# Kernel tuning notes

Hardware: AMD Instinct MI355X
Metric: run time of the kernel (lower is better)

The kernel has to match this reference:

```python
import jax, jax.numpy as jnp
import numpy as np

G, N_PER_G, V, H, DIN, DOUT, E = 1024, 64, 32, 128, 128, 10, 1048576
N = G * N_PER_G


def _lin(key, fan_in, fan_out):
    k1, k2 = jax.random.split(key)
    s = 1.0 / np.sqrt(fan_in)
    return (jax.random.uniform(k1, (fan_in, fan_out), jnp.float32, -s, s),
            jax.random.uniform(k2, (fan_out,), jnp.float32, -s, s))


def setup_inputs() -> dict:
    key = jax.random.key(0)
    ks = jax.random.split(key, 16)
    x = jax.random.normal(ks[0], (N, DIN), jnp.float32)
    # random edges constrained within each graph's contiguous node block
    gid = jax.random.randint(ks[1], (E,), 0, G)
    src = gid * N_PER_G + jax.random.randint(ks[2], (E,), 0, N_PER_G)
    dst = gid * N_PER_G + jax.random.randint(ks[3], (E,), 0, N_PER_G)
    edge_index = jnp.stack([src, dst]).astype(jnp.int64)
    batch = jnp.repeat(jnp.arange(G, dtype=jnp.int64), N_PER_G)
    edge_weights = jnp.ones((G, N_PER_G, V), jnp.float32) / V  # uniform init
    vemb = jax.random.normal(ks[4], (G, V, H), jnp.float32)
    vemb = vemb / jnp.linalg.norm(vemb, axis=-1, keepdims=True)
    W_emb, b_emb = _lin(ks[5], DIN, H)
    W_gcn, b_gcn = _lin(ks[6], H, H)
    aff_W1, aff_b1 = _lin(ks[7], H, H)
    aff_W2, aff_b2 = _lin(ks[8], H, H)
    vn_W1, vn_b1 = _lin(ks[9], H, H)
    vn_W2, vn_b2 = _lin(ks[10], H, H)
    mlp_W1, mlp_b1 = _lin(ks[11], H, H)
    mlp_W2, mlp_b2 = _lin(ks[12], H, DOUT)
    return dict(x=x, edge_index=edge_index, batch=batch, edge_weights=edge_weights,
                vemb=vemb, W_emb=W_emb, b_emb=b_emb, W_gcn=W_gcn, b_gcn=b_gcn,
                aff_W1=aff_W1, aff_b1=aff_b1, aff_W2=aff_W2, aff_b2=aff_b2,
                vn_W1=vn_W1, vn_b1=vn_b1, vn_W2=vn_W2, vn_b2=vn_b2,
                mlp_W1=mlp_W1, mlp_b1=mlp_b1, mlp_W2=mlp_W2, mlp_b2=mlp_b2)


def reference(x, edge_index, batch, edge_weights, vemb, W_emb, b_emb, W_gcn, b_gcn,
              aff_W1, aff_b1, aff_W2, aff_b2, vn_W1, vn_b1, vn_W2, vn_b2,
              mlp_W1, mlp_b1, mlp_W2, mlp_b2):
    n_nodes = x.shape[0]
    g, n, v = edge_weights.shape
    h = x @ W_emb + b_emb                                   # node embedding
    # GCNConv with self-loops and symmetric normalization
    hw = h @ W_gcn
    sl = jnp.arange(n_nodes)
    s = jnp.concatenate([edge_index[0], sl])
    d = jnp.concatenate([edge_index[1], sl])
    deg = jax.ops.segment_sum(jnp.ones_like(d, dtype=h.dtype), d, num_segments=n_nodes)
    inv = jax.lax.rsqrt(jnp.maximum(deg, 1.0))
    msg = hw[s] * (inv[s] * inv[d])[:, None]                # [E+N, H]
    h = jax.nn.relu(jax.ops.segment_sum(msg, d, num_segments=n_nodes) + b_gcn)
    # affinity MLP
    aff = jax.nn.relu(h @ aff_W1 + aff_b1) @ aff_W2 + aff_b2
    hg = h.reshape(g, n, -1)
    affg = aff.reshape(g, n, -1)
    # attention vs fixed normalized virtual-node embeddings
    att = jnp.einsum('gnh,gvh->gnv', affg, vemb) / jnp.sqrt(jnp.asarray(hg.shape[-1], h.dtype))
    ew = edge_weights * (1.0 + jax.nn.sigmoid(att))
    rs = ew.sum(axis=-1, keepdims=True)
    ew = ew / jnp.where(rs == 0, 1.0, rs)                   # row-normalize
    vn = jnp.einsum('gnv,gnh->gvh', ew, hg)                 # weighted scatter-pool
    vn = jax.nn.relu(vn @ vn_W1 + vn_b1) @ vn_W2 + vn_b2
    gf = vn.mean(axis=1)                                    # [G, H]
    return jax.nn.relu(gf @ mlp_W1 + mlp_b1) @ mlp_W2 + mlp_b2
```

## Files before the change

### kernel.cpp

```cpp
#include <hip/hip_runtime.h>
#include <hip/hip_bf16.h>
#include <cstddef>


#define EDGES 1048576
#define CAP 2048
#define SR 136
#define ST 72

typedef __attribute__((ext_vector_type(8))) short short8;
typedef __attribute__((ext_vector_type(4))) float f32x4;
typedef __hip_bfloat16 bf;
struct __align__(8) bf4 { bf v[4]; };

__global__ __launch_bounds__(256) void edge_hist(const int* __restrict__ ei,
                                                 unsigned* __restrict__ H)
{
    __shared__ unsigned lh[1024];
    int tid = threadIdx.x, b = blockIdx.x;
    for (int t = tid; t < 1024; t += 256) lh[t] = 0;
    __syncthreads();
    int base = b * 4096;
#pragma unroll 4
    for (int t = 0; t < 16; ++t) {
        int s = ei[base + t * 256 + tid];
        atomicAdd(&lh[s >> 6], 1u);
    }
    __syncthreads();
    for (int t = tid; t < 1024; t += 256) H[b * 1024 + t] = lh[t];
}

__global__ __launch_bounds__(256) void scan_conv(
    unsigned* __restrict__ H, unsigned* __restrict__ Tot,
    const float* __restrict__ w0, const float* __restrict__ w1,
    const float* __restrict__ w2, const float* __restrict__ w3,
    const float* __restrict__ w4, const float* __restrict__ w5,
    bf* __restrict__ outw)
{
    int b = blockIdx.x;
    if (b < 256) {
        int wv = threadIdx.x >> 6, lane = threadIdx.x & 63;
        int g = b * 4 + wv;
        unsigned v[4];
#pragma unroll
        for (int c = 0; c < 4; ++c) v[c] = H[(c * 64 + lane) * 1024 + g];
        unsigned run = 0;
#pragma unroll
        for (int c = 0; c < 4; ++c) {
            unsigned s = v[c];
            unsigned incl = s;
#pragma unroll
            for (int d = 1; d < 64; d <<= 1) {
                unsigned t = __shfl_up(incl, d);
                if (lane >= d) incl += t;
            }
            H[(c * 64 + lane) * 1024 + g] = run + (incl - s);
            run += __shfl(incl, 63);
        }
        if (lane == 0) Tot[g] = run;
    } else {
        int idx = (b - 256) * 256 + threadIdx.x;
        int n = idx >> 7, k = idx & 127;
        int off = (((n >> 4) * 4 + (k >> 5)) * 512) + (n & 15) * 32 + (k & 31);
        const float* srcs[6] = { w0, w1, w2, w3, w4, w5 };
#pragma unroll
        for (int m = 0; m < 6; ++m) {
            float vv = (m == 3) ? srcs[m][n * 128 + k] : srcs[m][k * 128 + n];
            outw[m * 16384 + off] = __float2bfloat16(vv);
        }
    }
}

__global__ __launch_bounds__(256) void edge_scatter(const int* __restrict__ ei,
                                                    const unsigned* __restrict__ H,
                                                    unsigned short* __restrict__ sorted)
{
    __shared__ unsigned lh[1024];
    __shared__ unsigned hrow[1024];
    int tid = threadIdx.x, b = blockIdx.x;
    for (int t = tid; t < 1024; t += 256) { lh[t] = 0; hrow[t] = H[b * 1024 + t]; }
    __syncthreads();
    int base = b * 4096;
    for (int t = 0; t < 16; ++t) {
        int e = base + t * 256 + tid;
        int s = ei[e], d = ei[EDGES + e];
        int g = s >> 6;
        unsigned r = atomicAdd(&lh[g], 1u);
        unsigned o = hrow[g] + r;
        if (o < (unsigned)CAP)
            sorted[(unsigned)g * CAP + o] = (unsigned short)(((d & 63) << 6) | (s & 63));
    }
}

__device__ __forceinline__ void loadB(const bf* __restrict__ gW, int wv, int l15,
                                      int kofs, short8* B)
{
#pragma unroll
    for (int nt = 0; nt < 2; ++nt)
#pragma unroll
        for (int ks = 0; ks < 4; ++ks)
            B[nt * 4 + ks] = *(const short8*)(gW + (((wv * 2 + nt) * 4 + ks) * 512)
                                              + l15 * 32 + kofs);
}

template<int MT, int KS, int SA>
__device__ __forceinline__ void mmaAB(const bf* sA, int rowA, int l15, int kofs,
                                      const short8* B, f32x4 (*acc)[2])
{
#pragma unroll
    for (int ks = 0; ks < KS; ++ks) {
        short8 a[MT];
#pragma unroll
        for (int m = 0; m < MT; ++m)
            a[m] = *(const short8*)(sA + (rowA + m * 16 + l15) * SA + ks * 32 + kofs);
#pragma unroll
        for (int m = 0; m < MT; ++m)
#pragma unroll
            for (int nt = 0; nt < 2; ++nt)
                acc[m][nt] = __builtin_amdgcn_mfma_f32_16x16x32_bf16(
                    a[m], B[nt * 4 + ks], acc[m][nt], 0, 0, 0);
    }
}

template<int MT, int KS, int SA, int SB>
__device__ __forceinline__ void mmaABlds(const bf* sA, int rowA, const bf* sB, int rowB,
                                         int l15, int kofs, f32x4 (*acc)[2])
{
#pragma unroll
    for (int ks = 0; ks < KS; ++ks) {
        short8 bb[2];
#pragma unroll
        for (int nt = 0; nt < 2; ++nt)
            bb[nt] = *(const short8*)(sB + (rowB + nt * 16 + l15) * SB + ks * 32 + kofs);
        short8 a[MT];
#pragma unroll
        for (int m = 0; m < MT; ++m)
            a[m] = *(const short8*)(sA + (rowA + m * 16 + l15) * SA + ks * 32 + kofs);
#pragma unroll
        for (int m = 0; m < MT; ++m)
#pragma unroll
            for (int nt = 0; nt < 2; ++nt)
                acc[m][nt] = __builtin_amdgcn_mfma_f32_16x16x32_bf16(
                    a[m], bb[nt], acc[m][nt], 0, 0, 0);
    }
}

__global__ __launch_bounds__(256, 2) void fused_graph(
    const float* __restrict__ x, const float* __restrict__ edge_w,
    const float* __restrict__ vemb, const bf* __restrict__ gWb,
    const float* __restrict__ b_emb,  const float* __restrict__ b_gcn,
    const float* __restrict__ aff_b1, const float* __restrict__ aff_b2,
    const float* __restrict__ vn_b1,  const float* __restrict__ vn_b2,
    const float* __restrict__ mlp_W1, const float* __restrict__ mlp_b1,
    const float* __restrict__ mlp_W2, const float* __restrict__ mlp_b2,
    const unsigned short* __restrict__ sorted,
    const unsigned* __restrict__ Tot,
    float* __restrict__ out)
{
    __shared__ __align__(16) bf sRM1[64 * SR];
    __shared__ __align__(16) bf sRM2[64 * SR];
    __shared__ __align__(16) bf sT1 [128 * ST];
    __shared__ __align__(16) bf sT2 [128 * ST];
    __shared__ __align__(16) bf sAdj[64 * ST];
    __shared__ float sInv[64];
    __shared__ float sBatt[32];

    unsigned* cnt = (unsigned*)sT1;
    bf* sVemb = sAdj;
    bf* sS    = sT1;
    bf* sEwnT = sT1 + 4608;
    float* sT2f = (float*)sT2;

    const int tid = threadIdx.x;
    const int g = blockIdx.x;
    const int wv = tid >> 6;
    const int lane = tid & 63;
    const int l15 = lane & 15;
    const int q = lane >> 4;
    const int kofs = q * 8;

    short8 Bp[8], Bn[8];
    loadB(gWb, wv, l15, kofs, Bp);
    loadB(gWb + 16384, wv, l15, kofs, Bn);
    float4 xreg[8];
    const float4* gx = (const float4*)(x + (size_t)g * 8192);
#pragma unroll
    for (int t = 0; t < 8; ++t) xreg[t] = gx[tid + t * 256];
    float4 vreg[4];
    const float4* gv = (const float4*)(vemb + (size_t)g * 4096);
#pragma unroll
    for (int t = 0; t < 4; ++t) vreg[t] = gv[tid + t * 256];
    float ewreg[2][4];
#pragma unroll
    for (int nt = 0; nt < 2; ++nt)
#pragma unroll
        for (int r = 0; r < 4; ++r)
            ewreg[nt][r] = edge_w[(size_t)g * 2048 + (wv * 16 + q * 4 + r) * 32
                                  + nt * 16 + l15];
    float bias_e[2], bias_g[2], bias_a1[2], bias_v1[2], bias_v2[2];
#pragma unroll
    for (int nt = 0; nt < 2; ++nt) {
        int n = wv * 32 + nt * 16 + l15;
        bias_e[nt] = b_emb[n];  bias_g[nt] = b_gcn[n]; bias_a1[nt] = aff_b1[n];
        bias_v1[nt] = vn_b1[n]; bias_v2[nt] = vn_b2[n];
    }
    unsigned ecnt = min(Tot[g], (unsigned)CAP);
    unsigned ebase = (unsigned)g * CAP;

#pragma unroll
    for (int t = 0; t < 4; ++t) cnt[tid * 4 + t] = 0u;
    __syncthreads();
    for (unsigned i = tid; i < ecnt; i += 256) {
        unsigned w = sorted[ebase + i];
        unsigned d = w >> 6, s = w & 63u;
        atomicAdd(&cnt[d * 16 + (s >> 2)], 1u << ((s & 3u) * 8));
    }
#pragma unroll
    for (int t = 0; t < 8; ++t) {
        int i = tid + t * 256;
        int row = i >> 5, c4 = i & 31;
        float4 w = xreg[t];
        bf4 tt;
        tt.v[0] = __float2bfloat16(w.x); tt.v[1] = __float2bfloat16(w.y);
        tt.v[2] = __float2bfloat16(w.z); tt.v[3] = __float2bfloat16(w.w);
        *(bf4*)(sRM1 + row * SR + c4 * 4) = tt;
    }
    __syncthreads();
    {
        int r = tid >> 2, q4 = tid & 3;
        float rs = 0.f;
#pragma unroll
        for (int t = 0; t < 4; ++t) {
            unsigned wd = cnt[r * 16 + q4 * 4 + t];
#pragma unroll
            for (int j = 0; j < 4; ++j) {
                int s = (q4 * 4 + t) * 4 + j;
                float v = (float)((wd >> (j * 8)) & 255u) + (s == r ? 1.f : 0.f);
                rs += v;
                sAdj[r * ST + s] = __float2bfloat16(v);
            }
        }
        rs += __shfl_xor(rs, 1);
        rs += __shfl_xor(rs, 2);
        if (q4 == 0) sInv[r] = rsqrtf(rs);
    }
    __syncthreads();

    {
        f32x4 acc[4][2] = {};
        mmaAB<4, 4, SR>(sRM1, 0, l15, kofs, Bp, acc);
        loadB(gWb + 2 * 16384, wv, l15, kofs, Bp);
#pragma unroll
        for (int m = 0; m < 4; ++m)
#pragma unroll
            for (int nt = 0; nt < 2; ++nt)
#pragma unroll
                for (int r = 0; r < 4; ++r)
                    sRM2[(m * 16 + q * 4 + r) * SR + wv * 32 + nt * 16 + l15] =
                        __float2bfloat16(acc[m][nt][r] + bias_e[nt]);
    }
    __syncthreads();

    {
        f32x4 acc[4][2] = {};
        mmaAB<4, 4, SR>(sRM2, 0, l15, kofs, Bn, acc);
        loadB(gWb + 3 * 16384, wv, l15, kofs, Bn);
#pragma unroll
        for (int m = 0; m < 4; ++m)
#pragma unroll
            for (int nt = 0; nt < 2; ++nt) {
                bf4 tv;
#pragma unroll
                for (int r = 0; r < 4; ++r)
                    tv.v[r] = __float2bfloat16(acc[m][nt][r] * sInv[m * 16 + q * 4 + r]);
                *(bf4*)(sT1 + (wv * 32 + nt * 16 + l15) * ST + m * 16 + q * 4) = tv;
            }
    }
    __syncthreads();

    {
        f32x4 acc[4][2] = {};
        mmaABlds<4, 2, ST, ST>(sAdj, 0, sT1, wv * 32, l15, kofs, acc);
#pragma unroll
        for (int m = 0; m < 4; ++m)
#pragma unroll
            for (int nt = 0; nt < 2; ++nt) {
                bf4 tv;
#pragma unroll
                for (int r = 0; r < 4; ++r) {
                    float v = fmaxf(acc[m][nt][r] * sInv[m * 16 + q * 4 + r] + bias_g[nt], 0.f);
                    sRM1[(m * 16 + q * 4 + r) * SR + wv * 32 + nt * 16 + l15] = __float2bfloat16(v);
                    tv.v[r] = __float2bfloat16(v);
                }
                *(bf4*)(sT2 + (wv * 32 + nt * 16 + l15) * ST + m * 16 + q * 4) = tv;
            }
    }
    __syncthreads();

    {
#pragma unroll
        for (int t = 0; t < 4; ++t) {
            int i = tid + t * 256;
            int v = i >> 5, o4 = i & 31;
            float4 w = vreg[t];
            bf4 tt;
            tt.v[0] = __float2bfloat16(w.x); tt.v[1] = __float2bfloat16(w.y);
            tt.v[2] = __float2bfloat16(w.z); tt.v[3] = __float2bfloat16(w.w);
            *(bf4*)(sVemb + v * SR + o4 * 4) = tt;
        }
        f32x4 acc[4][2] = {};
        mmaAB<4, 4, SR>(sRM1, 0, l15, kofs, Bp, acc);
        loadB(gWb + 4 * 16384, wv, l15, kofs, Bp);
#pragma unroll
        for (int m = 0; m < 4; ++m)
#pragma unroll
            for (int nt = 0; nt < 2; ++nt)
#pragma unroll
                for (int r = 0; r < 4; ++r)
                    sRM2[(m * 16 + q * 4 + r) * SR + wv * 32 + nt * 16 + l15] =
                        __float2bfloat16(fmaxf(acc[m][nt][r] + bias_a1[nt], 0.f));
    }
    __syncthreads();

    {
        f32x4 acc[2][2] = {};
        mmaAB<2, 4, SR>(sVemb, 0, l15, kofs, Bn, acc);
        loadB(gWb + 5 * 16384, wv, l15, kofs, Bn);
#pragma unroll
        for (int m = 0; m < 2; ++m)
#pragma unroll
            for (int nt = 0; nt < 2; ++nt)
#pragma unroll
                for (int r = 0; r < 4; ++r)
                    sS[(m * 16 + q * 4 + r) * SR + wv * 32 + nt * 16 + l15] =
                        __float2bfloat16(acc[m][nt][r]);
        int v = tid >> 3, sg = tid & 7;
        float s = 0.f;
        const bf* pv = sVemb + v * SR + sg * 16;
        const float* pb = aff_b2 + sg * 16;
#pragma unroll
        for (int o = 0; o < 16; ++o) s += pb[o] * __bfloat162float(pv[o]);
        s += __shfl_xor(s, 1); s += __shfl_xor(s, 2); s += __shfl_xor(s, 4);
        if (sg == 0) sBatt[v] = s;
    }
    __syncthreads();

    {
        f32x4 acc[1][2] = {};
        mmaABlds<1, 4, SR, SR>(sRM2, wv * 16, sS, 0, l15, kofs, acc);
        const float sc = 0.08838834764831845f;
        float bt[2] = { sBatt[l15], sBatt[16 + l15] };
        float e[2][4];
#pragma unroll
        for (int r = 0; r < 4; ++r) {
#pragma unroll
            for (int nt = 0; nt < 2; ++nt) {
                float att = (acc[0][nt][r] + bt[nt]) * sc;
                e[nt][r] = ewreg[nt][r] * (1.f + 1.f / (1.f + __expf(-att)));
            }
            float rs = e[0][r] + e[1][r];
            rs += __shfl_xor(rs, 1); rs += __shfl_xor(rs, 2);
            rs += __shfl_xor(rs, 4); rs += __shfl_xor(rs, 8);
            float ri = 1.f / rs;
            e[0][r] *= ri; e[1][r] *= ri;
        }
#pragma unroll
        for (int nt = 0; nt < 2; ++nt) {
            bf4 tv;
#pragma unroll
            for (int r = 0; r < 4; ++r) tv.v[r] = __float2bfloat16(e[nt][r]);
            *(bf4*)(sEwnT + (nt * 16 + l15) * ST + wv * 16 + q * 4) = tv;
        }
    }
    __syncthreads();

    {
        f32x4 acc[2][2] = {};
        mmaABlds<2, 2, ST, ST>(sEwnT, 0, sT2, wv * 32, l15, kofs, acc);
#pragma unroll
        for (int m = 0; m < 2; ++m)
#pragma unroll
            for (int nt = 0; nt < 2; ++nt)
#pragma unroll
                for (int r = 0; r < 4; ++r)
                    sRM1[(m * 16 + q * 4 + r) * SR + wv * 32 + nt * 16 + l15] =
                        __float2bfloat16(acc[m][nt][r]);
    }
    __syncthreads();

    {
        f32x4 acc[2][2] = {};
        mmaAB<2, 4, SR>(sRM1, 0, l15, kofs, Bp, acc);
#pragma unroll
        for (int m = 0; m < 2; ++m)
#pragma unroll
            for (int nt = 0; nt < 2; ++nt)
#pragma unroll
                for (int r = 0; r < 4; ++r)
                    sRM1[(32 + m * 16 + q * 4 + r) * SR + wv * 32 + nt * 16 + l15] =
                        __float2bfloat16(fmaxf(acc[m][nt][r] + bias_v1[nt], 0.f));
    }
    __syncthreads();

    {
        f32x4 acc[2][2] = {};
        mmaAB<2, 4, SR>(sRM1 + 32 * SR, 0, l15, kofs, Bn, acc);
#pragma unroll
        for (int m = 0; m < 2; ++m)
#pragma unroll
            for (int nt = 0; nt < 2; ++nt)
#pragma unroll
                for (int r = 0; r < 4; ++r)
                    sT2f[(wv * 32 + nt * 16 + l15) * 34 + m * 16 + q * 4 + r] =
                        acc[m][nt][r] + bias_v2[nt];
    }
    __syncthreads();

    float* sF = (float*)sRM2;
    if (tid < 128) {
        float s = 0.f;
#pragma unroll
        for (int v = 0; v < 32; ++v) s += sT2f[tid * 34 + v];
        sF[tid] = s * 0.03125f;
    }
    __syncthreads();

    {
        int o = tid & 127, hh = tid >> 7;
        const float* w = mlp_W1 + (size_t)(hh * 64) * 128 + o;
        float a = 0.f;
#pragma unroll 8
        for (int k = 0; k < 64; ++k) a = fmaf(sF[hh * 64 + k], w[k * 128], a);
        sF[128 + tid] = a;
    }
    __syncthreads();
    if (tid < 128)
        sF[384 + tid] = fmaxf(sF[128 + tid] + sF[256 + tid] + mlp_b1[tid], 0.f);
    __syncthreads();

    if (tid < 80) {
        int oo = tid >> 3, jg = tid & 7;
        float p = 0.f;
#pragma unroll
        for (int t2 = 0; t2 < 16; ++t2) {
            int j = jg * 16 + t2;
            p = fmaf(sF[384 + j], mlp_W2[j * 10 + oo], p);
        }
        p += __shfl_xor(p, 1); p += __shfl_xor(p, 2); p += __shfl_xor(p, 4);
        if (jg == 0) out[g * 10 + oo] = p + mlp_b2[oo];
    }
}

extern "C" void kernel_launch(void* const* d_in, const int* in_sizes, int n_in,
                              void* d_out, int out_size, void* d_ws, size_t ws_size,
                              hipStream_t stream)
{
    const float* x       = (const float*)d_in[0];
    const int*   ei      = (const int*)  d_in[1];
    const float* edge_w  = (const float*)d_in[3];
    const float* vemb    = (const float*)d_in[4];
    const float* W_emb   = (const float*)d_in[5];
    const float* b_emb   = (const float*)d_in[6];
    const float* W_gcn   = (const float*)d_in[7];
    const float* b_gcn   = (const float*)d_in[8];
    const float* aff_W1  = (const float*)d_in[9];
    const float* aff_b1  = (const float*)d_in[10];
    const float* aff_W2  = (const float*)d_in[11];
    const float* aff_b2  = (const float*)d_in[12];
    const float* vn_W1   = (const float*)d_in[13];
    const float* vn_b1   = (const float*)d_in[14];
    const float* vn_W2   = (const float*)d_in[15];
    const float* vn_b2   = (const float*)d_in[16];
    const float* mlp_W1  = (const float*)d_in[17];
    const float* mlp_b1  = (const float*)d_in[18];
    const float* mlp_W2  = (const float*)d_in[19];
    const float* mlp_b2  = (const float*)d_in[20];

    char* ws = (char*)d_ws;
    unsigned short* sorted = (unsigned short*)ws;
    unsigned* H    = (unsigned*)(ws + (4u << 20));
    unsigned* Tot  = (unsigned*)(ws + (5u << 20));
    bf*       gWb  = (bf*)      (ws + (5u << 20) + 65536);

    edge_hist  <<<dim3(256), dim3(256), 0, stream>>>(ei, H);
    scan_conv  <<<dim3(320), dim3(256), 0, stream>>>(
        H, Tot, W_emb, W_gcn, aff_W1, aff_W2, vn_W1, vn_W2, gWb);
    edge_scatter<<<dim3(256),dim3(256), 0, stream>>>(ei, H, sorted);
    fused_graph<<<dim3(1024), dim3(256), 0, stream>>>(
        x, edge_w, vemb, gWb, b_emb, b_gcn, aff_b1, aff_b2,
        vn_b1, vn_b2, mlp_W1, mlp_b1, mlp_W2, mlp_b2,
        sorted, Tot, (float*)d_out);
}
```

Before: 182.0 us.

## Split fused graph kernel across 8 waves with one N-tile per wave

The per-graph fused kernel now runs with 512 threads (8 waves) instead of 256. Each wave owns a single 16-column output tile rather than two, which halves the B-fragment registers, the accumulators and the per-thread loads. The attention row-normalisation now needs a cross-wave partial-sum exchange through shared memory plus an extra barrier, and the final MLP reduction is split four ways. The aim is more waves in flight and lower register pressure, at the cost of more synchronisation and less MFMA work per wave.

```diff
diff --git a/kernel.cpp b/kernel.cpp
--- a/kernel.cpp
+++ b/kernel.cpp
@@ -96,16 +96,13 @@
                                       int kofs, short8* B)
 {
 #pragma unroll
-    for (int nt = 0; nt < 2; ++nt)
-#pragma unroll
-        for (int ks = 0; ks < 4; ++ks)
-            B[nt * 4 + ks] = *(const short8*)(gW + (((wv * 2 + nt) * 4 + ks) * 512)
-                                              + l15 * 32 + kofs);
+    for (int ks = 0; ks < 4; ++ks)
+        B[ks] = *(const short8*)(gW + (wv * 4 + ks) * 512 + l15 * 32 + kofs);
 }
 
 template<int MT, int KS, int SA>
 __device__ __forceinline__ void mmaAB(const bf* sA, int rowA, int l15, int kofs,
-                                      const short8* B, f32x4 (*acc)[2])
+                                      const short8* B, f32x4* acc)
 {
 #pragma unroll
     for (int ks = 0; ks < KS; ++ks) {
@@ -115,37 +112,28 @@
             a[m] = *(const short8*)(sA + (rowA + m * 16 + l15) * SA + ks * 32 + kofs);
 #pragma unroll
         for (int m = 0; m < MT; ++m)
-#pragma unroll
-            for (int nt = 0; nt < 2; ++nt)
-                acc[m][nt] = __builtin_amdgcn_mfma_f32_16x16x32_bf16(
-                    a[m], B[nt * 4 + ks], acc[m][nt], 0, 0, 0);
+            acc[m] = __builtin_amdgcn_mfma_f32_16x16x32_bf16(a[m], B[ks], acc[m], 0, 0, 0);
     }
 }
 
 template<int MT, int KS, int SA, int SB>
 __device__ __forceinline__ void mmaABlds(const bf* sA, int rowA, const bf* sB, int rowB,
-                                         int l15, int kofs, f32x4 (*acc)[2])
+                                         int l15, int kofs, f32x4* acc)
 {
 #pragma unroll
     for (int ks = 0; ks < KS; ++ks) {
-        short8 bb[2];
-#pragma unroll
-        for (int nt = 0; nt < 2; ++nt)
-            bb[nt] = *(const short8*)(sB + (rowB + nt * 16 + l15) * SB + ks * 32 + kofs);
+        short8 bb = *(const short8*)(sB + (rowB + l15) * SB + ks * 32 + kofs);
         short8 a[MT];
 #pragma unroll
         for (int m = 0; m < MT; ++m)
             a[m] = *(const short8*)(sA + (rowA + m * 16 + l15) * SA + ks * 32 + kofs);
 #pragma unroll
         for (int m = 0; m < MT; ++m)
-#pragma unroll
-            for (int nt = 0; nt < 2; ++nt)
-                acc[m][nt] = __builtin_amdgcn_mfma_f32_16x16x32_bf16(
-                    a[m], bb[nt], acc[m][nt], 0, 0, 0);
-    }
-}
-
-__global__ __launch_bounds__(256, 2) void fused_graph(
+            acc[m] = __builtin_amdgcn_mfma_f32_16x16x32_bf16(a[m], bb, acc[m], 0, 0, 0);
+    }
+}
+
+__global__ __launch_bounds__(512, 4) void fused_graph(
     const float* __restrict__ x, const float* __restrict__ edge_w,
     const float* __restrict__ vemb, const bf* __restrict__ gWb,
     const float* __restrict__ b_emb,  const float* __restrict__ b_gcn,
@@ -167,6 +155,7 @@
 
     unsigned* cnt = (unsigned*)sT1;
     bf* sVemb = sAdj;
+    float* sPart = (float*)(sAdj + 4352);
     bf* sS    = sT1;
     bf* sEwnT = sT1 + 4608;
     float* sT2f = (float*)sT2;
@@ -178,46 +167,41 @@
     const int l15 = lane & 15;
     const int q = lane >> 4;
     const int kofs = q * 8;
-
-    short8 Bp[8], Bn[8];
+    const int c = wv * 16 + l15;
+
+    short8 Bp[4], Bn[4];
     loadB(gWb, wv, l15, kofs, Bp);
     loadB(gWb + 16384, wv, l15, kofs, Bn);
-    float4 xreg[8];
+    float4 xreg[4];
     const float4* gx = (const float4*)(x + (size_t)g * 8192);
 #pragma unroll
-    for (int t = 0; t < 8; ++t) xreg[t] = gx[tid + t * 256];
-    float4 vreg[4];
+    for (int t = 0; t < 4; ++t) xreg[t] = gx[tid + t * 512];
+    float4 vreg[2];
     const float4* gv = (const float4*)(vemb + (size_t)g * 4096);
 #pragma unroll
-    for (int t = 0; t < 4; ++t) vreg[t] = gv[tid + t * 256];
-    float ewreg[2][4];
-#pragma unroll
-    for (int nt = 0; nt < 2; ++nt)
-#pragma unroll
-        for (int r = 0; r < 4; ++r)
-            ewreg[nt][r] = edge_w[(size_t)g * 2048 + (wv * 16 + q * 4 + r) * 32
-                                  + nt * 16 + l15];
-    float bias_e[2], bias_g[2], bias_a1[2], bias_v1[2], bias_v2[2];
-#pragma unroll
-    for (int nt = 0; nt < 2; ++nt) {
-        int n = wv * 32 + nt * 16 + l15;
-        bias_e[nt] = b_emb[n];  bias_g[nt] = b_gcn[n]; bias_a1[nt] = aff_b1[n];
-        bias_v1[nt] = vn_b1[n]; bias_v2[nt] = vn_b2[n];
-    }
+    for (int t = 0; t < 2; ++t) vreg[t] = gv[tid + t * 512];
+    const int p6row = (wv & 3) * 16;
+    const int p6v   = (wv >> 2) * 16 + l15;
+    float ewreg[4];
+#pragma unroll
+    for (int r = 0; r < 4; ++r)
+        ewreg[r] = edge_w[(size_t)g * 2048 + (p6row + q * 4 + r) * 32 + p6v];
+    float bias_e = b_emb[c], bias_g = b_gcn[c], bias_a1 = aff_b1[c];
+    float bias_v1 = vn_b1[c], bias_v2 = vn_b2[c];
     unsigned ecnt = min(Tot[g], (unsigned)CAP);
     unsigned ebase = (unsigned)g * CAP;
 
 #pragma unroll
-    for (int t = 0; t < 4; ++t) cnt[tid * 4 + t] = 0u;
-    __syncthreads();
-    for (unsigned i = tid; i < ecnt; i += 256) {
+    for (int t = 0; t < 2; ++t) cnt[tid * 2 + t] = 0u;
+    __syncthreads();
+    for (unsigned i = tid; i < ecnt; i += 512) {
         unsigned w = sorted[ebase + i];
         unsigned d = w >> 6, s = w & 63u;
         atomicAdd(&cnt[d * 16 + (s >> 2)], 1u << ((s & 3u) * 8));
     }
 #pragma unroll
-    for (int t = 0; t < 8; ++t) {
-        int i = tid + t * 256;
+    for (int t = 0; t < 4; ++t) {
+        int i = tid + t * 512;
         int row = i >> 5, c4 = i & 31;
         float4 w = xreg[t];
         bf4 tt;
@@ -227,14 +211,14 @@
     }
     __syncthreads();
     {
-        int r = tid >> 2, q4 = tid & 3;
+        int r = tid >> 3, q8 = tid & 7;
         float rs = 0.f;
 #pragma unroll
-        for (int t = 0; t < 4; ++t) {
-            unsigned wd = cnt[r * 16 + q4 * 4 + t];
+        for (int t = 0; t < 2; ++t) {
+            unsigned wd = cnt[r * 16 + q8 * 2 + t];
 #pragma unroll
             for (int j = 0; j < 4; ++j) {
-                int s = (q4 * 4 + t) * 4 + j;
+                int s = (q8 * 2 + t) * 4 + j;
                 float v = (float)((wd >> (j * 8)) & 255u) + (s == r ? 1.f : 0.f);
                 rs += v;
                 sAdj[r * ST + s] = __float2bfloat16(v);
@@ -242,65 +226,60 @@
         }
         rs += __shfl_xor(rs, 1);
         rs += __shfl_xor(rs, 2);
-        if (q4 == 0) sInv[r] = rsqrtf(rs);
-    }
-    __syncthreads();
-
-    {
-        f32x4 acc[4][2] = {};
+        rs += __shfl_xor(rs, 4);
+        if (q8 == 0) sInv[r] = rsqrtf(rs);
+    }
+    __syncthreads();
+
+    {
+        f32x4 acc[4] = {};
         mmaAB<4, 4, SR>(sRM1, 0, l15, kofs, Bp, acc);
         loadB(gWb + 2 * 16384, wv, l15, kofs, Bp);
 #pragma unroll
         for (int m = 0; m < 4; ++m)
 #pragma unroll
-            for (int nt = 0; nt < 2; ++nt)
-#pragma unroll
-                for (int r = 0; r < 4; ++r)
-                    sRM2[(m * 16 + q * 4 + r) * SR + wv * 32 + nt * 16 + l15] =
-                        __float2bfloat16(acc[m][nt][r] + bias_e[nt]);
-    }
-    __syncthreads();
-
-    {
-        f32x4 acc[4][2] = {};
+            for (int r = 0; r < 4; ++r)
+                sRM2[(m * 16 + q * 4 + r) * SR + c] =
+                    __float2bfloat16(acc[m][r] + bias_e);
+    }
+    __syncthreads();
+
+    {
+        f32x4 acc[4] = {};
         mmaAB<4, 4, SR>(sRM2, 0, l15, kofs, Bn, acc);
         loadB(gWb + 3 * 16384, wv, l15, kofs, Bn);
 #pragma unroll
-        for (int m = 0; m < 4; ++m)
-#pragma unroll
-            for (int nt = 0; nt < 2; ++nt) {
-                bf4 tv;
-#pragma unroll
-                for (int r = 0; r < 4; ++r)
-                    tv.v[r] = __float2bfloat16(acc[m][nt][r] * sInv[m * 16 + q * 4 + r]);
-                *(bf4*)(sT1 + (wv * 32 + nt * 16 + l15) * ST + m * 16 + q * 4) = tv;
+        for (int m = 0; m < 4; ++m) {
+            bf4 tv;
+#pragma unroll
+            for (int r = 0; r < 4; ++r)
+                tv.v[r] = __float2bfloat16(acc[m][r] * sInv[m * 16 + q * 4 + r]);
+            *(bf4*)(sT1 + c * ST + m * 16 + q * 4) = tv;
+        }
+    }
+    __syncthreads();
+
+    {
+        f32x4 acc[4] = {};
+        mmaABlds<4, 2, ST, ST>(sAdj, 0, sT1, wv * 16, l15, kofs, acc);
+#pragma unroll
+        for (int m = 0; m < 4; ++m) {
+            bf4 tv;
+#pragma unroll
+            for (int r = 0; r < 4; ++r) {
+                float v = fmaxf(acc[m][r] * sInv[m * 16 + q * 4 + r] + bias_g, 0.f);
+                sRM1[(m * 16 + q * 4 + r) * SR + c] = __float2bfloat16(v);
+                tv.v[r] = __float2bfloat16(v);
             }
-    }
-    __syncthreads();
-
-    {
-        f32x4 acc[4][2] = {};
-        mmaABlds<4, 2, ST, ST>(sAdj, 0, sT1, wv * 32, l15, kofs, acc);
-#pragma unroll
-        for (int m = 0; m < 4; ++m)
-#pragma unroll
-            for (int nt = 0; nt < 2; ++nt) {
-                bf4 tv;
-#pragma unroll
-                for (int r = 0; r < 4; ++r) {
-                    float v = fmaxf(acc[m][nt][r] * sInv[m * 16 + q * 4 + r] + bias_g[nt], 0.f);
-                    sRM1[(m * 16 + q * 4 + r) * SR + wv * 32 + nt * 16 + l15] = __float2bfloat16(v);
-                    tv.v[r] = __float2bfloat16(v);
-                }
-                *(bf4*)(sT2 + (wv * 32 + nt * 16 + l15) * ST + m * 16 + q * 4) = tv;
-            }
-    }
-    __syncthreads();
-
-    {
-#pragma unroll
-        for (int t = 0; t < 4; ++t) {
-            int i = tid + t * 256;
+            *(bf4*)(sT2 + c * ST + m * 16 + q * 4) = tv;
+        }
+    }
+    __syncthreads();
+
+    {
+#pragma unroll
+        for (int t = 0; t < 2; ++t) {
+            int i = tid + t * 512;
             int v = i >> 5, o4 = i & 31;
             float4 w = vreg[t];
             bf4 tt;
@@ -308,111 +287,103 @@
             tt.v[2] = __float2bfloat16(w.z); tt.v[3] = __float2bfloat16(w.w);
             *(bf4*)(sVemb + v * SR + o4 * 4) = tt;
         }
-        f32x4 acc[4][2] = {};
+        f32x4 acc[4] = {};
         mmaAB<4, 4, SR>(sRM1, 0, l15, kofs, Bp, acc);
         loadB(gWb + 4 * 16384, wv, l15, kofs, Bp);
 #pragma unroll
         for (int m = 0; m < 4; ++m)
 #pragma unroll
-            for (int nt = 0; nt < 2; ++nt)
-#pragma unroll
-                for (int r = 0; r < 4; ++r)
-                    sRM2[(m * 16 + q * 4 + r) * SR + wv * 32 + nt * 16 + l15] =
-                        __float2bfloat16(fmaxf(acc[m][nt][r] + bias_a1[nt], 0.f));
-    }
-    __syncthreads();
-
-    {
-        f32x4 acc[2][2] = {};
+            for (int r = 0; r < 4; ++r)
+                sRM2[(m * 16 + q * 4 + r) * SR + c] =
+                    __float2bfloat16(fmaxf(acc[m][r] + bias_a1, 0.f));
+    }
+    __syncthreads();
+
+    {
+        f32x4 acc[2] = {};
         mmaAB<2, 4, SR>(sVemb, 0, l15, kofs, Bn, acc);
         loadB(gWb + 5 * 16384, wv, l15, kofs, Bn);
 #pragma unroll
         for (int m = 0; m < 2; ++m)
 #pragma unroll
-            for (int nt = 0; nt < 2; ++nt)
-#pragma unroll
-                for (int r = 0; r < 4; ++r)
-                    sS[(m * 16 + q * 4 + r) * SR + wv * 32 + nt * 16 + l15] =
-                        __float2bfloat16(acc[m][nt][r]);
-        int v = tid >> 3, sg = tid & 7;
-        float s = 0.f;
-        const bf* pv = sVemb + v * SR + sg * 16;
-        const float* pb = aff_b2 + sg * 16;
-#pragma unroll
-        for (int o = 0; o < 16; ++o) s += pb[o] * __bfloat162float(pv[o]);
-        s += __shfl_xor(s, 1); s += __shfl_xor(s, 2); s += __shfl_xor(s, 4);
-        if (sg == 0) sBatt[v] = s;
-    }
-    __syncthreads();
-
-    {
-        f32x4 acc[1][2] = {};
-        mmaABlds<1, 4, SR, SR>(sRM2, wv * 16, sS, 0, l15, kofs, acc);
+            for (int r = 0; r < 4; ++r)
+                sS[(m * 16 + q * 4 + r) * SR + c] = __float2bfloat16(acc[m][r]);
+        if (tid < 256) {
+            int v = tid >> 3, sg = tid & 7;
+            float s = 0.f;
+            const bf* pv = sVemb + v * SR + sg * 16;
+            const float* pb = aff_b2 + sg * 16;
+#pragma unroll
+            for (int o = 0; o < 16; ++o) s += pb[o] * __bfloat162float(pv[o]);
+            s += __shfl_xor(s, 1); s += __shfl_xor(s, 2); s += __shfl_xor(s, 4);
+            if (sg == 0) sBatt[v] = s;
+        }
+    }
+    __syncthreads();
+
+    {
+        f32x4 acc = {};
+        const int hv = wv >> 2;
+#pragma unroll
+        for (int ks = 0; ks < 4; ++ks) {
+            short8 bb = *(const short8*)(sS + (hv * 16 + l15) * SR + ks * 32 + kofs);
+            short8 a  = *(const short8*)(sRM2 + (p6row + l15) * SR + ks * 32 + kofs);
+            acc = __builtin_amdgcn_mfma_f32_16x16x32_bf16(a, bb, acc, 0, 0, 0);
+        }
         const float sc = 0.08838834764831845f;
-        float bt[2] = { sBatt[l15], sBatt[16 + l15] };
-        float e[2][4];
+        float bt = sBatt[p6v];
+        float e[4];
 #pragma unroll
         for (int r = 0; r < 4; ++r) {
-#pragma unroll
-            for (int nt = 0; nt < 2; ++nt) {
-                float att = (acc[0][nt][r] + bt[nt]) * sc;
-                e[nt][r] = ewreg[nt][r] * (1.f + 1.f / (1.f + __expf(-att)));
-            }
-            float rs = e[0][r] + e[1][r];
+            float att = (acc[r] + bt) * sc;
+            e[r] = ewreg[r] * (1.f + 1.f / (1.f + __expf(-att)));
+            float rs = e[r];
             rs += __shfl_xor(rs, 1); rs += __shfl_xor(rs, 2);
             rs += __shfl_xor(rs, 4); rs += __shfl_xor(rs, 8);
-            float ri = 1.f / rs;
-            e[0][r] *= ri; e[1][r] *= ri;
-        }
-#pragma unroll
-        for (int nt = 0; nt < 2; ++nt) {
-            bf4 tv;
-#pragma unroll
-            for (int r = 0; r < 4; ++r) tv.v[r] = __float2bfloat16(e[nt][r]);
-            *(bf4*)(sEwnT + (nt * 16 + l15) * ST + wv * 16 + q * 4) = tv;
-        }
-    }
-    __syncthreads();
-
-    {
-        f32x4 acc[2][2] = {};
-        mmaABlds<2, 2, ST, ST>(sEwnT, 0, sT2, wv * 32, l15, kofs, acc);
+            if (l15 == 0) sPart[hv * 64 + p6row + q * 4 + r] = rs;
+        }
+        __syncthreads();
+        bf4 tv;
+#pragma unroll
+        for (int r = 0; r < 4; ++r) {
+            float rs = sPart[p6row + q * 4 + r] + sPart[64 + p6row + q * 4 + r];
+            tv.v[r] = __float2bfloat16(e[r] / rs);
+        }
+        *(bf4*)(sEwnT + (hv * 16 + l15) * ST + p6row + q * 4) = tv;
+    }
+    __syncthreads();
+
+    {
+        f32x4 acc[2] = {};
+        mmaABlds<2, 2, ST, ST>(sEwnT, 0, sT2, wv * 16, l15, kofs, acc);
 #pragma unroll
         for (int m = 0; m < 2; ++m)
 #pragma unroll
-            for (int nt = 0; nt < 2; ++nt)
-#pragma unroll
-                for (int r = 0; r < 4; ++r)
-                    sRM1[(m * 16 + q * 4 + r) * SR + wv * 32 + nt * 16 + l15] =
-                        __float2bfloat16(acc[m][nt][r]);
-    }
-    __syncthreads();
-
-    {
-        f32x4 acc[2][2] = {};
+            for (int r = 0; r < 4; ++r)
+                sRM1[(m * 16 + q * 4 + r) * SR + c] = __float2bfloat16(acc[m][r]);
+    }
+    __syncthreads();
+
+    {
+        f32x4 acc[2] = {};
         mmaAB<2, 4, SR>(sRM1, 0, l15, kofs, Bp, acc);
 #pragma unroll
         for (int m = 0; m < 2; ++m)
 #pragma unroll
-            for (int nt = 0; nt < 2; ++nt)
-#pragma unroll
-                for (int r = 0; r < 4; ++r)
-                    sRM1[(32 + m * 16 + q * 4 + r) * SR + wv * 32 + nt * 16 + l15] =
-                        __float2bfloat16(fmaxf(acc[m][nt][r] + bias_v1[nt], 0.f));
-    }
-    __syncthreads();
-
-    {
-        f32x4 acc[2][2] = {};
+            for (int r = 0; r < 4; ++r)
+                sRM1[(32 + m * 16 + q * 4 + r) * SR + c] =
+                    __float2bfloat16(fmaxf(acc[m][r] + bias_v1, 0.f));
+    }
+    __syncthreads();
+
+    {
+        f32x4 acc[2] = {};
         mmaAB<2, 4, SR>(sRM1 + 32 * SR, 0, l15, kofs, Bn, acc);
 #pragma unroll
         for (int m = 0; m < 2; ++m)
 #pragma unroll
-            for (int nt = 0; nt < 2; ++nt)
-#pragma unroll
-                for (int r = 0; r < 4; ++r)
-                    sT2f[(wv * 32 + nt * 16 + l15) * 34 + m * 16 + q * 4 + r] =
-                        acc[m][nt][r] + bias_v2[nt];
+            for (int r = 0; r < 4; ++r)
+                sT2f[c * 34 + m * 16 + q * 4 + r] = acc[m][r] + bias_v2;
     }
     __syncthreads();
 
@@ -427,15 +398,16 @@
 
     {
         int o = tid & 127, hh = tid >> 7;
-        const float* w = mlp_W1 + (size_t)(hh * 64) * 128 + o;
+        const float* w = mlp_W1 + (size_t)(hh * 32) * 128 + o;
         float a = 0.f;
 #pragma unroll 8
-        for (int k = 0; k < 64; ++k) a = fmaf(sF[hh * 64 + k], w[k * 128], a);
-        sF[128 + tid] = a;
+        for (int k = 0; k < 32; ++k) a = fmaf(sF[hh * 32 + k], w[k * 128], a);
+        sF[128 + hh * 128 + o] = a;
     }
     __syncthreads();
     if (tid < 128)
-        sF[384 + tid] = fmaxf(sF[128 + tid] + sF[256 + tid] + mlp_b1[tid], 0.f);
+        sF[640 + tid] = fmaxf(sF[128 + tid] + sF[256 + tid] + sF[384 + tid]
+                              + sF[512 + tid] + mlp_b1[tid], 0.f);
     __syncthreads();
 
     if (tid < 80) {
@@ -444,7 +416,7 @@
 #pragma unroll
         for (int t2 = 0; t2 < 16; ++t2) {
             int j = jg * 16 + t2;
-            p = fmaf(sF[384 + j], mlp_W2[j * 10 + oo], p);
+            p = fmaf(sF[640 + j], mlp_W2[j * 10 + oo], p);
         }
         p += __shfl_xor(p, 1); p += __shfl_xor(p, 2); p += __shfl_xor(p, 4);
         if (jg == 0) out[g * 10 + oo] = p + mlp_b2[oo];
@@ -486,7 +458,7 @@
     scan_conv  <<<dim3(320), dim3(256), 0, stream>>>(
         H, Tot, W_emb, W_gcn, aff_W1, aff_W2, vn_W1, vn_W2, gWb);
     edge_scatter<<<dim3(256),dim3(256), 0, stream>>>(ei, H, sorted);
-    fused_graph<<<dim3(1024), dim3(256), 0, stream>>>(
+    fused_graph<<<dim3(1024), dim3(512), 0, stream>>>(
         x, edge_w, vemb, gWb, b_emb, b_gcn, aff_b1, aff_b2,
         vn_b1, vn_b2, mlp_W1, mlp_b1, mlp_W2, mlp_b2,
         sorted, Tot, (float*)d_out);
```

After: 195.5 us. +7.4%, slower.
